# Optimization experiments

Measured on AMD Instinct MI355X. Metric: run time of the kernel, lower is better.

## Reference

```python
import jax, jax.numpy as jnp
import numpy as np

N_NODES = 100000
N_EDGES = 600000
N_GRAPHS = 64


def _segment_mean(x, seg_ids, num_segments):
    s = jax.ops.segment_sum(x, seg_ids, num_segments=num_segments)
    cnt = jax.ops.segment_sum(jnp.ones((x.shape[0],), x.dtype), seg_ids, num_segments=num_segments)
    return s / jnp.maximum(cnt, 1.0)[:, None]


def _sage_conv(x, src, dst, W_l, W_r, b):
    # PyG SAGEConv (mean aggr): out = lin_l(mean_{j->i} x_j) + lin_r(x_i)
    mean_nb = _segment_mean(x[src], dst, x.shape[0])  # [N, d_in]
    return mean_nb @ W_l.T + x @ W_r.T + b


def setup_inputs() -> dict:
    key = jax.random.key(0)
    ks = jax.random.split(key, 16)
    bert_cls = jax.random.normal(ks[0], (N_GRAPHS, 768), jnp.float32)
    node_x = jax.random.normal(ks[1], (N_NODES, 128), jnp.float32)
    edge_index = jax.random.randint(ks[2], (2, N_EDGES), 0, N_NODES, jnp.int64 if jax.config.jax_enable_x64 else jnp.int32)
    batch_ids = jnp.sort(jax.random.randint(ks[3], (N_NODES,), 0, N_GRAPHS))
    s = 0.05
    return {
        'bert_cls': bert_cls,
        'node_x': node_x,
        'edge_index': edge_index,
        'batch_ids': batch_ids,
        'W_adapt': jax.random.normal(ks[4], (64, 768), jnp.float32) * s,
        'b_adapt': jnp.zeros((64,), jnp.float32),
        'W1l': jax.random.normal(ks[5], (64, 128), jnp.float32) * s,
        'W1r': jax.random.normal(ks[6], (64, 128), jnp.float32) * s,
        'b1': jnp.zeros((64,), jnp.float32),
        'W2l': jax.random.normal(ks[7], (16, 64), jnp.float32) * s,
        'W2r': jax.random.normal(ks[8], (16, 64), jnp.float32) * s,
        'b2': jnp.zeros((16,), jnp.float32),
        'Wm': jax.random.normal(ks[9], (16, 16), jnp.float32) * s,
        'bm': jnp.zeros((16,), jnp.float32),
    }


def reference(bert_cls, node_x, edge_index, batch_ids,
              W_adapt, b_adapt, W1l, W1r, b1, W2l, W2r, b2, Wm, bm):
    # pooled BERT CLS -> adaptive linear (forward() applies no relu here)
    last_state = bert_cls @ W_adapt.T + b_adapt  # [bs, 64]

    src, dst = edge_index[0], edge_index[1]
    h = jax.nn.relu(_sage_conv(node_x, src, dst, W1l, W1r, b1))  # [N, 64]
    h = _sage_conv(h, src, dst, W2l, W2r, b2)                    # [N, 16]

    graph_emb = _segment_mean(h, batch_ids, N_GRAPHS)            # [bs, 16]
    graph_emb = graph_emb @ Wm.T + bm

    return jnp.concatenate([last_state, graph_emb], axis=-1)     # [bs, 80]
```

## Files before the change

### kernel.cpp

```cpp
#include <hip/hip_runtime.h>

#define N_NODES 100000
#define N_EDGES 600000
#define N_GRAPHS 64


__global__ void k_count(const int* __restrict__ dst, int* __restrict__ deg) {
    int e = blockIdx.x * 256 + threadIdx.x;
    if (e < N_EDGES) atomicAdd(&deg[dst[e]], 1);
}

__global__ void k_scan1(const int* __restrict__ deg, int* __restrict__ offs,
                        int* __restrict__ bsums) {
    __shared__ int s[256];
    int t = threadIdx.x, b = blockIdx.x;
    int base = b * 1024 + t * 4;
    int v0 = (base + 0 < N_NODES) ? deg[base + 0] : 0;
    int v1 = (base + 1 < N_NODES) ? deg[base + 1] : 0;
    int v2 = (base + 2 < N_NODES) ? deg[base + 2] : 0;
    int v3 = (base + 3 < N_NODES) ? deg[base + 3] : 0;
    int tsum = v0 + v1 + v2 + v3;
    s[t] = tsum;
    __syncthreads();
    for (int o = 1; o < 256; o <<= 1) {
        int x = (t >= o) ? s[t - o] : 0;
        __syncthreads();
        s[t] += x;
        __syncthreads();
    }
    int p = s[t] - tsum;
    if (base + 0 < N_NODES) offs[base + 0] = p;
    p += v0;
    if (base + 1 < N_NODES) offs[base + 1] = p;
    p += v1;
    if (base + 2 < N_NODES) offs[base + 2] = p;
    p += v2;
    if (base + 3 < N_NODES) offs[base + 3] = p;
    if (t == 255) bsums[b] = s[255];
}

__global__ void k_scan2(const int* __restrict__ bsums, int* __restrict__ boff) {
    __shared__ int s[128];
    int t = threadIdx.x;
    int nb = (N_NODES + 1023) / 1024;
    int v = (t < nb) ? bsums[t] : 0;
    s[t] = v;
    __syncthreads();
    for (int o = 1; o < 128; o <<= 1) {
        int x = (t >= o) ? s[t - o] : 0;
        __syncthreads();
        s[t] += x;
        __syncthreads();
    }
    boff[t] = s[t] - v;
}

__global__ void k_scan3(int* __restrict__ offs, const int* __restrict__ boff,
                        int* __restrict__ cursor) {
    int i = blockIdx.x * 256 + threadIdx.x;
    if (i < N_NODES) {
        int v = offs[i] + boff[i >> 10];
        offs[i] = v;
        cursor[i] = v;
    }
}

__global__ void k_fill(const int* __restrict__ src, const int* __restrict__ dst,
                       int* __restrict__ cursor, int* __restrict__ ssrc) {
    int e = blockIdx.x * 256 + threadIdx.x;
    if (e < N_EDGES) {
        int d = dst[e];
        int pos = atomicAdd(&cursor[d], 1);
        ssrc[pos] = src[e];
    }
}

__global__ void k_prepack(const float* __restrict__ W1l, const float* __restrict__ W1r,
                          const float* __restrict__ W2l, const float* __restrict__ W2r,
                          float* __restrict__ Pg, float* __restrict__ P2g) {
    int i = blockIdx.x * 256 + threadIdx.x;
    if (i < 16384) {
        int k = i >> 7, d = i & 127;
        Pg[i] = (d < 64) ? W1l[d * 128 + k] : W1r[(d - 64) * 128 + k];
    } else if (i < 18432) {
        int j = i - 16384, k = j >> 5, d = j & 31;
        P2g[j] = (d < 16) ? W2l[d * 64 + k] : W2r[(d - 16) * 64 + k];
    }
}


#define KC 32
#define LDP 132

__launch_bounds__(256, 4)
__global__ void k_xform1(const float* __restrict__ x, const float* __restrict__ Pg,
                         float* __restrict__ xl, float* __restrict__ xr) {
    __shared__ float At[KC * LDP];
    __shared__ float Bt[KC * LDP];
    int tid = threadIdx.x;
    int wave = tid >> 6, lane = tid & 63;
    int wr = wave >> 1, wc = wave & 1;
    int li = lane >> 3, lj = lane & 7;
    int tbase = blockIdx.x * 128;
    const float4* x4 = (const float4*)x;
    const float4* Pg4 = (const float4*)Pg;

    float4 av[4], bv[4];
#pragma unroll
    for (int u = 0; u < 4; ++u) {
        int idx = u * 256 + tid;
        int n = idx >> 3, q = idx & 7;
        int node = min(tbase + n, N_NODES - 1);
        av[u] = x4[node * 32 + q];
        bv[u] = Pg4[idx];
    }
    float acc[8][8];
#pragma unroll
    for (int i = 0; i < 8; ++i)
#pragma unroll
        for (int j = 0; j < 8; ++j) acc[i][j] = 0.f;

    for (int k0 = 0; k0 < 128; k0 += KC) {
#pragma unroll
        for (int u = 0; u < 4; ++u) {
            int idx = u * 256 + tid;
            int n = idx >> 3, q = idx & 7;
            int ns = n ^ ((q & 7) << 3);
            At[(4 * q + 0) * LDP + ns] = av[u].x;
            At[(4 * q + 1) * LDP + ns] = av[u].y;
            At[(4 * q + 2) * LDP + ns] = av[u].z;
            At[(4 * q + 3) * LDP + ns] = av[u].w;
            int kk = idx >> 5, q2 = idx & 31;
            *(float4*)&Bt[kk * LDP + 4 * q2] = bv[u];
        }
        __syncthreads();
        if (k0 + KC < 128) {
#pragma unroll
            for (int u = 0; u < 4; ++u) {
                int idx = u * 256 + tid;
                int n = idx >> 3, q = idx & 7;
                int node = min(tbase + n, N_NODES - 1);
                av[u] = x4[node * 32 + ((k0 + KC) >> 2) + q];
                bv[u] = Pg4[(k0 + KC) * 32 + idx];
            }
        }
#pragma unroll 4
        for (int kk = 0; kk < KC; ++kk) {
            float a[8], b[8];
            int lia = (li ^ ((kk >> 2) & 7)) * 8;
            *(float4*)&a[0] = *(const float4*)&At[kk * LDP + wr * 64 + lia];
            *(float4*)&a[4] = *(const float4*)&At[kk * LDP + wr * 64 + lia + 4];
            *(float4*)&b[0] = *(const float4*)&Bt[kk * LDP + wc * 64 + lj * 8];
            *(float4*)&b[4] = *(const float4*)&Bt[kk * LDP + wc * 64 + lj * 8 + 4];
#pragma unroll
            for (int i = 0; i < 8; ++i)
#pragma unroll
                for (int j = 0; j < 8; ++j)
                    acc[i][j] = fmaf(a[i], b[j], acc[i][j]);
        }
        __syncthreads();
    }
    float* outb = wc ? xr : xl;
#pragma unroll
    for (int i = 0; i < 8; ++i) {
        int node = tbase + wr * 64 + li * 8 + i;
        if (node < N_NODES) {
            float4* p = (float4*)(outb + node * 64 + lj * 8);
            p[0] = make_float4(acc[i][0], acc[i][1], acc[i][2], acc[i][3]);
            p[1] = make_float4(acc[i][4], acc[i][5], acc[i][6], acc[i][7]);
        }
    }
}


__launch_bounds__(256)
__global__ void k_gather1(const float* __restrict__ xl, const int* __restrict__ ssrc,
                          const int* __restrict__ offs, const int* __restrict__ deg,
                          const float* __restrict__ b1, float* __restrict__ h1) {
    int tid = blockIdx.x * 256 + threadIdx.x;
    int wid = tid >> 6, lane = tid & 63;
    int nWaves = (gridDim.x * 256) >> 6;
    float bias = b1[lane];

    int node = wid;
    if (node >= N_NODES) return;
    int o = offs[node], dg = deg[node];
    float self = h1[node * 64 + lane];
    while (true) {
        int nnode = node + nWaves;
        int no = 0, ndg = 0;
        float nself = 0.f;
        if (nnode < N_NODES) {
            no = offs[nnode];
            ndg = deg[nnode];
            nself = h1[nnode * 64 + lane];
        }
        int os = __builtin_amdgcn_readfirstlane(o);
        int ds = __builtin_amdgcn_readfirstlane(dg);
        float a0 = 0.f, a1 = 0.f, a2 = 0.f, a3 = 0.f;
        float a4 = 0.f, a5 = 0.f, a6 = 0.f, a7 = 0.f;
        int last = ds - 1;
        for (int u = 0; u < ds; u += 8) {
            int n0 = ssrc[os + u];
            int n1 = ssrc[os + min(u + 1, last)];
            int n2 = ssrc[os + min(u + 2, last)];
            int n3 = ssrc[os + min(u + 3, last)];
            int n4 = ssrc[os + min(u + 4, last)];
            int n5 = ssrc[os + min(u + 5, last)];
            int n6 = ssrc[os + min(u + 6, last)];
            int n7 = ssrc[os + min(u + 7, last)];
            float v0 = xl[n0 * 64 + lane];
            float v1 = xl[n1 * 64 + lane];
            float v2 = xl[n2 * 64 + lane];
            float v3 = xl[n3 * 64 + lane];
            float v4 = xl[n4 * 64 + lane];
            float v5 = xl[n5 * 64 + lane];
            float v6 = xl[n6 * 64 + lane];
            float v7 = xl[n7 * 64 + lane];
            a0 += v0;
            a1 = fmaf(v1, (u + 1 < ds) ? 1.f : 0.f, a1);
            a2 = fmaf(v2, (u + 2 < ds) ? 1.f : 0.f, a2);
            a3 = fmaf(v3, (u + 3 < ds) ? 1.f : 0.f, a3);
            a4 = fmaf(v4, (u + 4 < ds) ? 1.f : 0.f, a4);
            a5 = fmaf(v5, (u + 5 < ds) ? 1.f : 0.f, a5);
            a6 = fmaf(v6, (u + 6 < ds) ? 1.f : 0.f, a6);
            a7 = fmaf(v7, (u + 7 < ds) ? 1.f : 0.f, a7);
        }
        float inv = 1.f / (float)max(ds, 1);
        float mean = (((a0 + a1) + (a2 + a3)) + ((a4 + a5) + (a6 + a7))) * inv;
        h1[node * 64 + lane] = fmaxf(self + bias + mean, 0.f);
        if (nnode >= N_NODES) break;
        node = nnode;
        o = no;
        dg = ndg;
        self = nself;
    }
}


#define LD2 68

__launch_bounds__(256)
__global__ void k_xform2(const float* __restrict__ h1, const float* __restrict__ P2g,
                         float* __restrict__ h1l, float* __restrict__ h2pre) {
    __shared__ float S[64 * LD2];
    int tid = threadIdx.x;
    int wave = __builtin_amdgcn_readfirstlane(tid >> 6);
    int lane = tid & 63;
    int tbase = blockIdx.x * 64;
    const float4* h4 = (const float4*)h1;

    for (int idx = tid; idx < 64 * 16; idx += 256) {
        int n = idx >> 4, q = idx & 15;
        int node = min(tbase + n, N_NODES - 1);
        *(float4*)&S[n * LD2 + 4 * q] = h4[node * 16 + q];
    }
    __syncthreads();

    int node = tbase + lane;
    int dbase = wave * 8;
    float acc[8] = {0.f, 0.f, 0.f, 0.f, 0.f, 0.f, 0.f, 0.f};
    const float* Sn = S + lane * LD2;
#pragma unroll 4
    for (int k4 = 0; k4 < 16; ++k4) {
        float4 s = *(const float4*)&Sn[4 * k4];
        const float* Wk = P2g + (4 * k4) * 32 + dbase;
#pragma unroll
        for (int c = 0; c < 4; ++c) {
            float sv = (c == 0) ? s.x : (c == 1) ? s.y : (c == 2) ? s.z : s.w;
            const float* W = Wk + c * 32;
#pragma unroll
            for (int dd = 0; dd < 8; ++dd)
                acc[dd] = fmaf(W[dd], sv, acc[dd]);
        }
    }
    if (node < N_NODES) {
        float4 lo = make_float4(acc[0], acc[1], acc[2], acc[3]);
        float4 hi = make_float4(acc[4], acc[5], acc[6], acc[7]);
        if (wave < 2) {
            float4* p = (float4*)(h1l + node * 16 + wave * 8);
            p[0] = lo;
            p[1] = hi;
        } else {
            float4* p = (float4*)(h2pre + node * 16 + (wave - 2) * 8);
            p[0] = lo;
            p[1] = hi;
        }
    }
}


__launch_bounds__(256)
__global__ void k_g2pool(const float* __restrict__ h1l, const float* __restrict__ h2pre,
                         const int* __restrict__ ssrc, const int* __restrict__ offs,
                         const int* __restrict__ deg, const int* __restrict__ batch,
                         const float* __restrict__ b2,
                         float* __restrict__ gsum, float* __restrict__ gcnt) {
    __shared__ float bins[N_GRAPHS][17];
    int tid = threadIdx.x;
    for (int i = tid; i < N_GRAPHS * 17; i += 256) ((float*)bins)[i] = 0.f;
    __syncthreads();

    int wave = tid >> 6, lane = tid & 63;
    int sub = lane >> 4, d = lane & 15;
    float bias = b2[d];

    int chunk = (N_NODES + gridDim.x - 1) / gridDim.x;
    int cs = blockIdx.x * chunk;
    int ce = min(N_NODES, cs + chunk);

    for (int base = cs + wave * 4; base < ce; base += 16) {
        int node = base + sub;
        bool valid = node < ce;
        int nn = valid ? node : cs;
        int o = offs[nn], dg = deg[nn];
        float a0 = 0.f, a1 = 0.f, a2 = 0.f, a3 = 0.f;
        int last = dg - 1;
        for (int u = 0; u < dg; u += 4) {
            int n0 = ssrc[o + u];
            int n1 = ssrc[o + min(u + 1, last)];
            int n2 = ssrc[o + min(u + 2, last)];
            int n3 = ssrc[o + min(u + 3, last)];
            float v0 = h1l[n0 * 16 + d];
            float v1 = h1l[n1 * 16 + d];
            float v2 = h1l[n2 * 16 + d];
            float v3 = h1l[n3 * 16 + d];
            float m1 = (u + 1 < dg) ? 1.f : 0.f;
            float m2 = (u + 2 < dg) ? 1.f : 0.f;
            float m3 = (u + 3 < dg) ? 1.f : 0.f;
            a0 += v0;
            a1 = fmaf(v1, m1, a1);
            a2 = fmaf(v2, m2, a2);
            a3 = fmaf(v3, m3, a3);
        }
        float inv = 1.f / (float)max(dg, 1);
        float val = h2pre[nn * 16 + d] + bias + ((a0 + a1) + (a2 + a3)) * inv;
        if (valid) {
            int g = batch[nn];
            atomicAdd(&bins[g][d], val);
            if (d == 0) atomicAdd(&bins[g][16], 1.f);
        }
    }
    __syncthreads();
    for (int i = tid; i < N_GRAPHS * 17; i += 256) {
        int g = i / 17, c = i - g * 17;
        float v = bins[g][c];
        if (v != 0.f) {
            if (c < 16) atomicAdd(&gsum[g * 16 + c], v);
            else        atomicAdd(&gcnt[g], v);
        }
    }
}


__global__ void k_final(const float* __restrict__ bert, const float* __restrict__ Wad,
                        const float* __restrict__ bad, const float* __restrict__ Wm,
                        const float* __restrict__ bm, const float* __restrict__ gsum,
                        const float* __restrict__ gcnt, float* __restrict__ out) {
    int g = blockIdx.x;
    int t = threadIdx.x;
    if (t < 64) {
        const float4* br = (const float4*)(bert + g * 768);
        const float4* wr = (const float4*)(Wad + t * 768);
        float acc = bad[t];
#pragma unroll 8
        for (int k = 0; k < 192; ++k) {
            float4 bv = br[k], wv = wr[k];
            acc += bv.x * wv.x + bv.y * wv.y + bv.z * wv.z + bv.w * wv.w;
        }
        out[g * 80 + t] = acc;
    } else if (t < 80) {
        int j = t - 64;
        float ic = 1.f / fmaxf(gcnt[g], 1.f);
        float acc = bm[j];
#pragma unroll
        for (int k = 0; k < 16; ++k) acc += Wm[j * 16 + k] * gsum[g * 16 + k] * ic;
        out[g * 80 + t] = acc;
    }
}

extern "C" void kernel_launch(void* const* d_in, const int* in_sizes, int n_in,
                              void* d_out, int out_size, void* d_ws, size_t ws_size,
                              hipStream_t stream) {
    const float* bert   = (const float*)d_in[0];
    const float* node_x = (const float*)d_in[1];
    const int*   edge   = (const int*)d_in[2];
    const int*   batch  = (const int*)d_in[3];
    const float* Wad    = (const float*)d_in[4];
    const float* bad    = (const float*)d_in[5];
    const float* W1l    = (const float*)d_in[6];
    const float* W1r    = (const float*)d_in[7];
    const float* b1     = (const float*)d_in[8];
    const float* W2l    = (const float*)d_in[9];
    const float* W2r    = (const float*)d_in[10];
    const float* b2     = (const float*)d_in[11];
    const float* Wm     = (const float*)d_in[12];
    const float* bm     = (const float*)d_in[13];
    float* out = (float*)d_out;

    const int* src = edge;
    const int* dst = edge + N_EDGES;

    char* ws = (char*)d_ws;
    int*    deg    = (int*)(ws);
    int*    offs   = (int*)(ws + 400000);
    int*    cursor = (int*)(ws + 800000);
    int*    bsums  = (int*)(ws + 1200000);
    int*    boff   = (int*)(ws + 1200512);
    int*    ssrc   = (int*)(ws + 1201024);
    float*  xl     = (float*)(ws + 3601024);
    float*  h1     = (float*)(ws + 29201024);
    float*  Pg     = (float*)(ws + 54801024);
    float*  P2g    = (float*)(ws + 54866560);
    float*  gsum   = (float*)(ws + 54874752);
    float*  gcnt   = (float*)(ws + 54878848);
    float*  h1l    = (float*)(ws + 3601024);
    float*  h2pre  = (float*)(ws + 10001024);

    hipMemsetAsync(deg, 0, 400000, stream);
    hipMemsetAsync(gsum, 0, 4096 + 256, stream);

    k_count<<<(N_EDGES + 255) / 256, 256, 0, stream>>>(dst, deg);
    k_scan1<<<(N_NODES + 1023) / 1024, 256, 0, stream>>>(deg, offs, bsums);
    k_scan2<<<1, 128, 0, stream>>>(bsums, boff);
    k_scan3<<<(N_NODES + 255) / 256, 256, 0, stream>>>(offs, boff, cursor);
    k_fill<<<(N_EDGES + 255) / 256, 256, 0, stream>>>(src, dst, cursor, ssrc);
    k_prepack<<<72, 256, 0, stream>>>(W1l, W1r, W2l, W2r, Pg, P2g);

    int nT128 = (N_NODES + 127) / 128;
    int nT64  = (N_NODES + 63) / 64;
    k_xform1<<<nT128, 256, 0, stream>>>(node_x, Pg, xl, h1);
    k_gather1<<<2048, 256, 0, stream>>>(xl, ssrc, offs, deg, b1, h1);
    k_xform2<<<nT64, 256, 0, stream>>>(h1, P2g, h1l, h2pre);
    k_g2pool<<<512, 256, 0, stream>>>(h1l, h2pre, ssrc, offs, deg, batch, b2, gsum, gcnt);
    k_final<<<N_GRAPHS, 128, 0, stream>>>(bert, Wad, bad, Wm, bm, gsum, gcnt, out);
}
```

Measured before the change: 334.4 us.

## Shrink xform1 tile to 64 nodes, read weights from global, narrow gather unroll

```diff
diff --git a/kernel.cpp b/kernel.cpp
--- a/kernel.cpp
+++ b/kernel.cpp
@@ -89,81 +89,61 @@
 }
 
 
-#define KC 32
-#define LDP 132
-
-__launch_bounds__(256, 4)
+#define KC1 64
+#define LDA 68
+
+__launch_bounds__(128, 4)
 __global__ void k_xform1(const float* __restrict__ x, const float* __restrict__ Pg,
                          float* __restrict__ xl, float* __restrict__ xr) {
-    __shared__ float At[KC * LDP];
-    __shared__ float Bt[KC * LDP];
+    __shared__ float At[KC1 * LDA];
     int tid = threadIdx.x;
     int wave = tid >> 6, lane = tid & 63;
-    int wr = wave >> 1, wc = wave & 1;
     int li = lane >> 3, lj = lane & 7;
-    int tbase = blockIdx.x * 128;
+    int tbase = blockIdx.x * 64;
     const float4* x4 = (const float4*)x;
     const float4* Pg4 = (const float4*)Pg;
 
-    float4 av[4], bv[4];
-#pragma unroll
-    for (int u = 0; u < 4; ++u) {
-        int idx = u * 256 + tid;
-        int n = idx >> 3, q = idx & 7;
-        int node = min(tbase + n, N_NODES - 1);
-        av[u] = x4[node * 32 + q];
-        bv[u] = Pg4[idx];
-    }
     float acc[8][8];
 #pragma unroll
     for (int i = 0; i < 8; ++i)
 #pragma unroll
         for (int j = 0; j < 8; ++j) acc[i][j] = 0.f;
 
-    for (int k0 = 0; k0 < 128; k0 += KC) {
-#pragma unroll
-        for (int u = 0; u < 4; ++u) {
-            int idx = u * 256 + tid;
-            int n = idx >> 3, q = idx & 7;
-            int ns = n ^ ((q & 7) << 3);
-            At[(4 * q + 0) * LDP + ns] = av[u].x;
-            At[(4 * q + 1) * LDP + ns] = av[u].y;
-            At[(4 * q + 2) * LDP + ns] = av[u].z;
-            At[(4 * q + 3) * LDP + ns] = av[u].w;
-            int kk = idx >> 5, q2 = idx & 31;
-            *(float4*)&Bt[kk * LDP + 4 * q2] = bv[u];
+    for (int k0 = 0; k0 < 128; k0 += KC1) {
+        if (k0) __syncthreads();
+#pragma unroll
+        for (int u = 0; u < 8; ++u) {
+            int idx = u * 128 + tid;
+            int n = idx >> 4, q = idx & 15;
+            int node = min(tbase + n, N_NODES - 1);
+            float4 v = x4[node * 32 + (k0 >> 2) + q];
+            int col = 4 * ((n >> 2) ^ q) + (n & 3);
+            At[(4 * q + 0) * LDA + col] = v.x;
+            At[(4 * q + 1) * LDA + col] = v.y;
+            At[(4 * q + 2) * LDA + col] = v.z;
+            At[(4 * q + 3) * LDA + col] = v.w;
         }
         __syncthreads();
-        if (k0 + KC < 128) {
-#pragma unroll
-            for (int u = 0; u < 4; ++u) {
-                int idx = u * 256 + tid;
-                int n = idx >> 3, q = idx & 7;
-                int node = min(tbase + n, N_NODES - 1);
-                av[u] = x4[node * 32 + ((k0 + KC) >> 2) + q];
-                bv[u] = Pg4[(k0 + KC) * 32 + idx];
-            }
-        }
 #pragma unroll 4
-        for (int kk = 0; kk < KC; ++kk) {
+        for (int kk = 0; kk < KC1; ++kk) {
+            int key = kk >> 2;
             float a[8], b[8];
-            int lia = (li ^ ((kk >> 2) & 7)) * 8;
-            *(float4*)&a[0] = *(const float4*)&At[kk * LDP + wr * 64 + lia];
-            *(float4*)&a[4] = *(const float4*)&At[kk * LDP + wr * 64 + lia + 4];
-            *(float4*)&b[0] = *(const float4*)&Bt[kk * LDP + wc * 64 + lj * 8];
-            *(float4*)&b[4] = *(const float4*)&Bt[kk * LDP + wc * 64 + lj * 8 + 4];
+            *(float4*)&a[0] = *(const float4*)&At[kk * LDA + 4 * ((2 * li) ^ key)];
+            *(float4*)&a[4] = *(const float4*)&At[kk * LDA + 4 * ((2 * li + 1) ^ key)];
+            const float4* bp = Pg4 + (k0 + kk) * 32 + wave * 16 + lj * 2;
+            *(float4*)&b[0] = bp[0];
+            *(float4*)&b[4] = bp[1];
 #pragma unroll
             for (int i = 0; i < 8; ++i)
 #pragma unroll
                 for (int j = 0; j < 8; ++j)
                     acc[i][j] = fmaf(a[i], b[j], acc[i][j]);
         }
-        __syncthreads();
-    }
-    float* outb = wc ? xr : xl;
+    }
+    float* outb = wave ? xr : xl;
 #pragma unroll
     for (int i = 0; i < 8; ++i) {
-        int node = tbase + wr * 64 + li * 8 + i;
+        int node = tbase + li * 8 + i;
         if (node < N_NODES) {
             float4* p = (float4*)(outb + node * 64 + lj * 8);
             p[0] = make_float4(acc[i][0], acc[i][1], acc[i][2], acc[i][3]);
@@ -198,36 +178,23 @@
         int os = __builtin_amdgcn_readfirstlane(o);
         int ds = __builtin_amdgcn_readfirstlane(dg);
         float a0 = 0.f, a1 = 0.f, a2 = 0.f, a3 = 0.f;
-        float a4 = 0.f, a5 = 0.f, a6 = 0.f, a7 = 0.f;
         int last = ds - 1;
-        for (int u = 0; u < ds; u += 8) {
+        for (int u = 0; u < ds; u += 4) {
             int n0 = ssrc[os + u];
             int n1 = ssrc[os + min(u + 1, last)];
             int n2 = ssrc[os + min(u + 2, last)];
             int n3 = ssrc[os + min(u + 3, last)];
-            int n4 = ssrc[os + min(u + 4, last)];
-            int n5 = ssrc[os + min(u + 5, last)];
-            int n6 = ssrc[os + min(u + 6, last)];
-            int n7 = ssrc[os + min(u + 7, last)];
             float v0 = xl[n0 * 64 + lane];
             float v1 = xl[n1 * 64 + lane];
             float v2 = xl[n2 * 64 + lane];
             float v3 = xl[n3 * 64 + lane];
-            float v4 = xl[n4 * 64 + lane];
-            float v5 = xl[n5 * 64 + lane];
-            float v6 = xl[n6 * 64 + lane];
-            float v7 = xl[n7 * 64 + lane];
             a0 += v0;
             a1 = fmaf(v1, (u + 1 < ds) ? 1.f : 0.f, a1);
             a2 = fmaf(v2, (u + 2 < ds) ? 1.f : 0.f, a2);
             a3 = fmaf(v3, (u + 3 < ds) ? 1.f : 0.f, a3);
-            a4 = fmaf(v4, (u + 4 < ds) ? 1.f : 0.f, a4);
-            a5 = fmaf(v5, (u + 5 < ds) ? 1.f : 0.f, a5);
-            a6 = fmaf(v6, (u + 6 < ds) ? 1.f : 0.f, a6);
-            a7 = fmaf(v7, (u + 7 < ds) ? 1.f : 0.f, a7);
         }
         float inv = 1.f / (float)max(ds, 1);
-        float mean = (((a0 + a1) + (a2 + a3)) + ((a4 + a5) + (a6 + a7))) * inv;
+        float mean = ((a0 + a1) + (a2 + a3)) * inv;
         h1[node * 64 + lane] = fmaxf(self + bias + mean, 0.f);
         if (nnode >= N_NODES) break;
         node = nnode;
@@ -427,9 +394,8 @@
     k_fill<<<(N_EDGES + 255) / 256, 256, 0, stream>>>(src, dst, cursor, ssrc);
     k_prepack<<<72, 256, 0, stream>>>(W1l, W1r, W2l, W2r, Pg, P2g);
 
-    int nT128 = (N_NODES + 127) / 128;
-    int nT64  = (N_NODES + 63) / 64;
-    k_xform1<<<nT128, 256, 0, stream>>>(node_x, Pg, xl, h1);
+    int nT64 = (N_NODES + 63) / 64;
+    k_xform1<<<nT64, 128, 0, stream>>>(node_x, Pg, xl, h1);
     k_gather1<<<2048, 256, 0, stream>>>(xl, ssrc, offs, deg, b1, h1);
     k_xform2<<<nT64, 256, 0, stream>>>(h1, P2g, h1l, h2pre);
     k_g2pool<<<512, 256, 0, stream>>>(h1l, h2pre, ssrc, offs, deg, batch, b2, gsum, gcnt);
```

Result: no change. 332.8 us (-0.5%).

## Vectorize edge gathers with float4 lanes and simplify xform1 staging

Applied to the files above, without the earlier changes.

```diff
diff --git a/kernel.cpp b/kernel.cpp
--- a/kernel.cpp
+++ b/kernel.cpp
@@ -105,15 +105,6 @@
     const float4* x4 = (const float4*)x;
     const float4* Pg4 = (const float4*)Pg;
 
-    float4 av[4], bv[4];
-#pragma unroll
-    for (int u = 0; u < 4; ++u) {
-        int idx = u * 256 + tid;
-        int n = idx >> 3, q = idx & 7;
-        int node = min(tbase + n, N_NODES - 1);
-        av[u] = x4[node * 32 + q];
-        bv[u] = Pg4[idx];
-    }
     float acc[8][8];
 #pragma unroll
     for (int i = 0; i < 8; ++i)
@@ -121,35 +112,31 @@
         for (int j = 0; j < 8; ++j) acc[i][j] = 0.f;
 
     for (int k0 = 0; k0 < 128; k0 += KC) {
+        if (k0) __syncthreads();
 #pragma unroll
         for (int u = 0; u < 4; ++u) {
             int idx = u * 256 + tid;
             int n = idx >> 3, q = idx & 7;
-            int ns = n ^ ((q & 7) << 3);
-            At[(4 * q + 0) * LDP + ns] = av[u].x;
-            At[(4 * q + 1) * LDP + ns] = av[u].y;
-            At[(4 * q + 2) * LDP + ns] = av[u].z;
-            At[(4 * q + 3) * LDP + ns] = av[u].w;
-            int kk = idx >> 5, q2 = idx & 31;
-            *(float4*)&Bt[kk * LDP + 4 * q2] = bv[u];
+            int node = min(tbase + n, N_NODES - 1);
+            float4 v = x4[node * 32 + (k0 >> 2) + q];
+            At[(4 * q + 0) * LDP + n] = v.x;
+            At[(4 * q + 1) * LDP + n] = v.y;
+            At[(4 * q + 2) * LDP + n] = v.z;
+            At[(4 * q + 3) * LDP + n] = v.w;
+        }
+#pragma unroll
+        for (int u = 0; u < 4; ++u) {
+            int idx = u * 256 + tid;
+            int kk = idx >> 5, q = idx & 31;
+            float4 w = Pg4[(k0 + kk) * 32 + q];
+            *(float4*)&Bt[kk * LDP + 4 * q] = w;
         }
         __syncthreads();
-        if (k0 + KC < 128) {
-#pragma unroll
-            for (int u = 0; u < 4; ++u) {
-                int idx = u * 256 + tid;
-                int n = idx >> 3, q = idx & 7;
-                int node = min(tbase + n, N_NODES - 1);
-                av[u] = x4[node * 32 + ((k0 + KC) >> 2) + q];
-                bv[u] = Pg4[(k0 + KC) * 32 + idx];
-            }
-        }
 #pragma unroll 4
         for (int kk = 0; kk < KC; ++kk) {
             float a[8], b[8];
-            int lia = (li ^ ((kk >> 2) & 7)) * 8;
-            *(float4*)&a[0] = *(const float4*)&At[kk * LDP + wr * 64 + lia];
-            *(float4*)&a[4] = *(const float4*)&At[kk * LDP + wr * 64 + lia + 4];
+            *(float4*)&a[0] = *(const float4*)&At[kk * LDP + wr * 64 + li * 8];
+            *(float4*)&a[4] = *(const float4*)&At[kk * LDP + wr * 64 + li * 8 + 4];
             *(float4*)&b[0] = *(const float4*)&Bt[kk * LDP + wc * 64 + lj * 8];
             *(float4*)&b[4] = *(const float4*)&Bt[kk * LDP + wc * 64 + lj * 8 + 4];
 #pragma unroll
@@ -158,7 +145,6 @@
                 for (int j = 0; j < 8; ++j)
                     acc[i][j] = fmaf(a[i], b[j], acc[i][j]);
         }
-        __syncthreads();
     }
     float* outb = wc ? xr : xl;
 #pragma unroll
@@ -180,55 +166,53 @@
     int tid = blockIdx.x * 256 + threadIdx.x;
     int wid = tid >> 6, lane = tid & 63;
     int nWaves = (gridDim.x * 256) >> 6;
-    float bias = b1[lane];
+    int sub = lane >> 4, q = lane & 15;
+    float4 bias = ((const float4*)b1)[q];
+    const float4* xl4 = (const float4*)xl;
+    float4* h14 = (float4*)h1;
 
     int node = wid;
     if (node >= N_NODES) return;
     int o = offs[node], dg = deg[node];
-    float self = h1[node * 64 + lane];
+    float4 self = h14[node * 16 + q];
     while (true) {
         int nnode = node + nWaves;
         int no = 0, ndg = 0;
-        float nself = 0.f;
+        float4 nself = make_float4(0.f, 0.f, 0.f, 0.f);
         if (nnode < N_NODES) {
             no = offs[nnode];
             ndg = deg[nnode];
-            nself = h1[nnode * 64 + lane];
+            nself = h14[nnode * 16 + q];
         }
         int os = __builtin_amdgcn_readfirstlane(o);
         int ds = __builtin_amdgcn_readfirstlane(dg);
-        float a0 = 0.f, a1 = 0.f, a2 = 0.f, a3 = 0.f;
-        float a4 = 0.f, a5 = 0.f, a6 = 0.f, a7 = 0.f;
+        float ax = 0.f, ay = 0.f, az = 0.f, aw = 0.f;
         int last = ds - 1;
         for (int u = 0; u < ds; u += 8) {
-            int n0 = ssrc[os + u];
-            int n1 = ssrc[os + min(u + 1, last)];
-            int n2 = ssrc[os + min(u + 2, last)];
-            int n3 = ssrc[os + min(u + 3, last)];
-            int n4 = ssrc[os + min(u + 4, last)];
-            int n5 = ssrc[os + min(u + 5, last)];
-            int n6 = ssrc[os + min(u + 6, last)];
-            int n7 = ssrc[os + min(u + 7, last)];
-            float v0 = xl[n0 * 64 + lane];
-            float v1 = xl[n1 * 64 + lane];
-            float v2 = xl[n2 * 64 + lane];
-            float v3 = xl[n3 * 64 + lane];
-            float v4 = xl[n4 * 64 + lane];
-            float v5 = xl[n5 * 64 + lane];
-            float v6 = xl[n6 * 64 + lane];
-            float v7 = xl[n7 * 64 + lane];
-            a0 += v0;
-            a1 = fmaf(v1, (u + 1 < ds) ? 1.f : 0.f, a1);
-            a2 = fmaf(v2, (u + 2 < ds) ? 1.f : 0.f, a2);
-            a3 = fmaf(v3, (u + 3 < ds) ? 1.f : 0.f, a3);
-            a4 = fmaf(v4, (u + 4 < ds) ? 1.f : 0.f, a4);
-            a5 = fmaf(v5, (u + 5 < ds) ? 1.f : 0.f, a5);
-            a6 = fmaf(v6, (u + 6 < ds) ? 1.f : 0.f, a6);
-            a7 = fmaf(v7, (u + 7 < ds) ? 1.f : 0.f, a7);
-        }
+            int na = ssrc[os + min(u + sub, last)];
+            int nb = ssrc[os + min(u + 4 + sub, last)];
+            float4 va = xl4[na * 16 + q];
+            float4 vb = xl4[nb * 16 + q];
+            float ma = (u + sub < ds) ? 1.f : 0.f;
+            float mb = (u + 4 + sub < ds) ? 1.f : 0.f;
+            ax = fmaf(va.x, ma, ax); ay = fmaf(va.y, ma, ay);
+            az = fmaf(va.z, ma, az); aw = fmaf(va.w, ma, aw);
+            ax = fmaf(vb.x, mb, ax); ay = fmaf(vb.y, mb, ay);
+            az = fmaf(vb.z, mb, az); aw = fmaf(vb.w, mb, aw);
+        }
+        ax += __shfl_xor(ax, 16); ay += __shfl_xor(ay, 16);
+        az += __shfl_xor(az, 16); aw += __shfl_xor(aw, 16);
+        ax += __shfl_xor(ax, 32); ay += __shfl_xor(ay, 32);
+        az += __shfl_xor(az, 32); aw += __shfl_xor(aw, 32);
         float inv = 1.f / (float)max(ds, 1);
-        float mean = (((a0 + a1) + (a2 + a3)) + ((a4 + a5) + (a6 + a7))) * inv;
-        h1[node * 64 + lane] = fmaxf(self + bias + mean, 0.f);
+        if (sub == 0) {
+            float4 r;
+            r.x = fmaxf(self.x + bias.x + ax * inv, 0.f);
+            r.y = fmaxf(self.y + bias.y + ay * inv, 0.f);
+            r.z = fmaxf(self.z + bias.z + az * inv, 0.f);
+            r.w = fmaxf(self.w + bias.w + aw * inv, 0.f);
+            h14[node * 16 + q] = r;
+        }
         if (nnode >= N_NODES) break;
         node = nnode;
         o = no;
@@ -302,44 +286,47 @@
     __syncthreads();
 
     int wave = tid >> 6, lane = tid & 63;
-    int sub = lane >> 4, d = lane & 15;
-    float bias = b2[d];
+    int slot = lane >> 2, d4 = lane & 3;
+    float4 bias = ((const float4*)b2)[d4];
+    const float4* hl4 = (const float4*)h1l;
+    const float4* hp4 = (const float4*)h2pre;
 
     int chunk = (N_NODES + gridDim.x - 1) / gridDim.x;
     int cs = blockIdx.x * chunk;
     int ce = min(N_NODES, cs + chunk);
 
-    for (int base = cs + wave * 4; base < ce; base += 16) {
-        int node = base + sub;
-        bool valid = node < ce;
-        int nn = valid ? node : cs;
-        int o = offs[nn], dg = deg[nn];
-        float a0 = 0.f, a1 = 0.f, a2 = 0.f, a3 = 0.f;
-        int last = dg - 1;
-        for (int u = 0; u < dg; u += 4) {
-            int n0 = ssrc[o + u];
-            int n1 = ssrc[o + min(u + 1, last)];
-            int n2 = ssrc[o + min(u + 2, last)];
-            int n3 = ssrc[o + min(u + 3, last)];
-            float v0 = h1l[n0 * 16 + d];
-            float v1 = h1l[n1 * 16 + d];
-            float v2 = h1l[n2 * 16 + d];
-            float v3 = h1l[n3 * 16 + d];
-            float m1 = (u + 1 < dg) ? 1.f : 0.f;
-            float m2 = (u + 2 < dg) ? 1.f : 0.f;
-            float m3 = (u + 3 < dg) ? 1.f : 0.f;
-            a0 += v0;
-            a1 = fmaf(v1, m1, a1);
-            a2 = fmaf(v2, m2, a2);
-            a3 = fmaf(v3, m3, a3);
-        }
-        float inv = 1.f / (float)max(dg, 1);
-        float val = h2pre[nn * 16 + d] + bias + ((a0 + a1) + (a2 + a3)) * inv;
-        if (valid) {
-            int g = batch[nn];
-            atomicAdd(&bins[g][d], val);
-            if (d == 0) atomicAdd(&bins[g][16], 1.f);
-        }
+    for (int node = cs + wave; node < ce; node += 4) {
+        int os = __builtin_amdgcn_readfirstlane(offs[node]);
+        int ds = __builtin_amdgcn_readfirstlane(deg[node]);
+        float4 hp = hp4[node * 4 + d4];
+        float ax = 0.f, ay = 0.f, az = 0.f, aw = 0.f;
+        int last = ds - 1;
+        for (int u = 0; u < ds; u += 16) {
+            int n = ssrc[os + min(u + slot, last)];
+            float4 v = hl4[n * 4 + d4];
+            float m = (u + slot < ds) ? 1.f : 0.f;
+            ax = fmaf(v.x, m, ax); ay = fmaf(v.y, m, ay);
+            az = fmaf(v.z, m, az); aw = fmaf(v.w, m, aw);
+        }
+#pragma unroll
+        for (int off = 4; off <= 32; off <<= 1) {
+            ax += __shfl_xor(ax, off); ay += __shfl_xor(ay, off);
+            az += __shfl_xor(az, off); aw += __shfl_xor(aw, off);
+        }
+        float inv = 1.f / (float)max(ds, 1);
+        float4 val;
+        val.x = hp.x + bias.x + ax * inv;
+        val.y = hp.y + bias.y + ay * inv;
+        val.z = hp.z + bias.z + az * inv;
+        val.w = hp.w + bias.w + aw * inv;
+        int g = batch[node];
+        if (lane < 4) {
+            atomicAdd(&bins[g][4 * lane + 0], val.x);
+            atomicAdd(&bins[g][4 * lane + 1], val.y);
+            atomicAdd(&bins[g][4 * lane + 2], val.z);
+            atomicAdd(&bins[g][4 * lane + 3], val.w);
+        }
+        if (lane == 0) atomicAdd(&bins[g][16], 1.f);
     }
     __syncthreads();
     for (int i = tid; i < N_GRAPHS * 17; i += 256) {
```

Result: no change. 340.1 us (+1.7%).
